# Kernel tuning notes

Hardware: AMD Instinct MI355X
Metric: run time of the kernel (lower is better)

## Reference

```python
import jax, jax.numpy as jnp
import numpy as np

PATCH_SIZE = 16
HOP_DISTANCE = 7.0


def setup_inputs() -> dict:
    key = jax.random.key(0)
    x = jax.random.normal(key, (1, 1024, 1024), dtype=jnp.float32)
    return {"x": x}


def _patchify(x, p):
    # Faithful replication of F.unfold(kernel=p, stride=p) followed by .view(-1, p, p)
    # on the contiguous [1, C*p*p, L] unfold output (row-major reshape).
    C, H, W = x.shape
    nH, nW = H // p, W // p
    # unfold layout: [C*p*p, L] with element (c*p*p + ki*p + kj, bi*nW + bj)
    cols = x.reshape(C, nH, p, nW, p).transpose(0, 2, 4, 1, 3).reshape(C * p * p, nH * nW)
    # torch .view(-1, p, p) on contiguous [C*p*p, L] == row-major reshape
    return cols.reshape(-1, p, p)  # [N, p, p], N = C * nH * nW


def reference(x):
    p = PATCH_SIZE
    patches = _patchify(x, p)  # [N, p, p]
    # distance(patch_i, patch_j) = norm over dim=1 (rows) -> per-column vector of length p.
    # d2[i, j, k] = sum_r (patches[i, r, k] - patches[j, r, k])**2, via Gram trick.
    sq = jnp.sum(patches * patches, axis=1)                      # [N, p]
    G = jnp.einsum('irk,jrk->ijk', patches, patches)             # [N, N, p]
    d2 = jnp.maximum(sq[:, None, :] + sq[None, :, :] - 2.0 * G, 0.0)
    # A[i, j] = 1 iff all per-column norms <= hop_distance
    A = jnp.all(jnp.sqrt(d2) <= HOP_DISTANCE, axis=-1).astype(jnp.float32)  # [N, N]
    return A
```

## Files before the change

kernel.cpp:

```cpp
#include <hip/hip_runtime.h>


#define NPATCH 4096
#define BT 64
#define KC 2
#define NPH 8

__global__ __launch_bounds__(128, 2) void adj_kernel(const float* __restrict__ x,
                                                     float* __restrict__ A) {
#pragma clang fp contract(off)
    __shared__ float4 Si[BT][8];
    __shared__ float4 Sj[BT][8];
    __shared__ float sqs[2][KC][BT];

    int t = blockIdx.x;
    int bi = (int)((sqrtf(8.0f * (float)t + 1.0f) - 1.0f) * 0.5f);
    while ((bi + 1) * (bi + 2) / 2 <= t) ++bi;
    while (bi * (bi + 1) / 2 > t) --bi;
    int bj = t - bi * (bi + 1) / 2;

    const int i0 = bi * BT;
    const int j0 = bj * BT;
    const int tid = threadIdx.x;
    const int tx = tid & 15;
    const int ty = tid >> 4;

    unsigned int bad = 0u;

    for (int kp = 0; kp < NPH; ++kp) {
        __syncthreads();
#pragma unroll
        for (int l = 0; l < 8; ++l) {
            int gid = l * 128 + tid;
            int side = gid >> 9;
            int q = gid & 511;
            int kl = q & 1;
            int r = (q >> 1) & 15;
            int rl = q >> 5;
            int k = kp * KC + kl;
            int b = side ? bj : bi;
            int h = rl * 64 + (r >> 2) * 16 + (b >> 2);
            int w0 = (r & 3) * 256 + k * 16 + ((4 * b) & 15);
            float4 v = *(const float4*)&x[h * 1024 + w0];
            const float* vp = (const float*)&v;
            int c = (kl << 2) | (r >> 2);
            int e = r & 3;
            float4* Sb = side ? &Sj[0][0] : &Si[0][0];
#pragma unroll
            for (int dd = 0; dd < 4; ++dd) {
                int row = 16 * dd + rl;
                int ch = c ^ ((row >> 2) & 7);
                ((float*)&Sb[row * 8 + ch])[e] = vp[dd];
            }
        }
        __syncthreads();
#pragma unroll
        for (int p = 0; p < 2; ++p) {
            int s0 = p * 128 + tid;
            int side = s0 >> 7;
            int kl = (s0 >> 6) & 1;
            int row = s0 & 63;
            const float4* Sb = side ? &Sj[row][0] : &Si[row][0];
            int swz = (row >> 2) & 7;
            float acc;
            {
                float4 v = Sb[(kl * 4) ^ swz];
                acc = v.x * v.x;
                float t1 = v.y * v.y; acc = acc + t1;
                float t2 = v.z * v.z; acc = acc + t2;
                float t3 = v.w * v.w; acc = acc + t3;
            }
#pragma unroll
            for (int rc = 1; rc < 4; ++rc) {
                float4 v = Sb[(kl * 4 + rc) ^ swz];
                float t0 = v.x * v.x; acc = acc + t0;
                float t1 = v.y * v.y; acc = acc + t1;
                float t2 = v.z * v.z; acc = acc + t2;
                float t3 = v.w * v.w; acc = acc + t3;
            }
            sqs[side][kl][row] = acc;
        }
        __syncthreads();
#pragma unroll
        for (int kl = 0; kl < KC; ++kl) {
            float d[8][4];
#pragma unroll
            for (int u = 0; u < 8; ++u)
#pragma unroll
                for (int v = 0; v < 4; ++v) d[u][v] = 0.0f;
#pragma unroll
            for (int rc = 0; rc < 4; ++rc) {
                int c = kl * 4 + rc;
                float4 a[8], b[4];
#pragma unroll
                for (int u = 0; u < 8; ++u)
                    a[u] = Si[ty * 8 + u][c ^ ((2 * ty + (u >> 2)) & 7)];
#pragma unroll
                for (int v = 0; v < 4; ++v)
                    b[v] = Sj[tx * 4 + v][c ^ (tx & 7)];
#pragma unroll
                for (int u = 0; u < 8; ++u)
#pragma unroll
                    for (int v = 0; v < 4; ++v) {
                        d[u][v] = fmaf(a[u].x, b[v].x, d[u][v]);
                        d[u][v] = fmaf(a[u].y, b[v].y, d[u][v]);
                        d[u][v] = fmaf(a[u].z, b[v].z, d[u][v]);
                        d[u][v] = fmaf(a[u].w, b[v].w, d[u][v]);
                    }
            }
#pragma unroll
            for (int u = 0; u < 8; ++u) {
                float si = sqs[0][kl][ty * 8 + u];
#pragma unroll
                for (int v = 0; v < 4; ++v) {
                    float sj = sqs[1][kl][tx * 4 + v];
                    float s = si + sj;
                    float d2 = fmaf(-2.0f, d[u][v], s);
                    bad |= (d2 > 49.0f) ? (1u << (u * 4 + v)) : 0u;
                }
            }
        }
    }

#pragma unroll
    for (int u = 0; u < 8; ++u) {
        float4 o;
        o.x = (bad >> (u * 4 + 0)) & 1u ? 0.0f : 1.0f;
        o.y = (bad >> (u * 4 + 1)) & 1u ? 0.0f : 1.0f;
        o.z = (bad >> (u * 4 + 2)) & 1u ? 0.0f : 1.0f;
        o.w = (bad >> (u * 4 + 3)) & 1u ? 0.0f : 1.0f;
        *(float4*)&A[(size_t)(i0 + ty * 8 + u) * NPATCH + j0 + tx * 4] = o;
    }
    if (bi != bj) {
#pragma unroll
        for (int v = 0; v < 4; ++v) {
#pragma unroll
            for (int g = 0; g < 2; ++g) {
                float4 o;
                o.x = (bad >> ((g * 4 + 0) * 4 + v)) & 1u ? 0.0f : 1.0f;
                o.y = (bad >> ((g * 4 + 1) * 4 + v)) & 1u ? 0.0f : 1.0f;
                o.z = (bad >> ((g * 4 + 2) * 4 + v)) & 1u ? 0.0f : 1.0f;
                o.w = (bad >> ((g * 4 + 3) * 4 + v)) & 1u ? 0.0f : 1.0f;
                *(float4*)&A[(size_t)(j0 + tx * 4 + v) * NPATCH + i0 + ty * 8 + g * 4] = o;
            }
        }
    }
}

extern "C" void kernel_launch(void* const* d_in, const int* in_sizes, int n_in,
                              void* d_out, int out_size, void* d_ws, size_t ws_size,
                              hipStream_t stream) {
    const float* x = (const float*)d_in[0];
    float* A = (float*)d_out;
    (void)d_ws; (void)ws_size;

    const int nblk = (NPATCH / BT) * (NPATCH / BT + 1) / 2;
    adj_kernel<<<nblk, 128, 0, stream>>>(x, A);
}
```

Before: 185.2 us.

## Use 128x64 rectangular tiles over the triangular block grid with 256 threads

Enlarges each block's tile to 128 i-rows by 64 j-columns, with 256 threads. Blocks are mapped onto a triangular grid of 64-row strip pairs against 64-column strips, with adjusted index math and shared arrays. Each block loads three patch strips and reuses the j strip across two i strips, which cuts per-output shared loads and the block count. The mirrored store now always runs, so diagonal blocks write some elements twice, once directly and once transposed. Bigger tiles mean fewer blocks, which can affect tail balance.

```diff
diff --git a/kernel.cpp b/kernel.cpp
--- a/kernel.cpp
+++ b/kernel.cpp
@@ -2,25 +2,25 @@
 
 
 #define NPATCH 4096
-#define BT 64
 #define KC 2
 #define NPH 8
 
-__global__ __launch_bounds__(128, 2) void adj_kernel(const float* __restrict__ x,
+__global__ __launch_bounds__(256, 2) void adj_kernel(const float* __restrict__ x,
                                                      float* __restrict__ A) {
 #pragma clang fp contract(off)
-    __shared__ float4 Si[BT][8];
-    __shared__ float4 Sj[BT][8];
-    __shared__ float sqs[2][KC][BT];
+    __shared__ float4 Si[128][8];
+    __shared__ float4 Sj[64][8];
+    __shared__ float sqi[KC][128];
+    __shared__ float sqj[KC][64];
 
     int t = blockIdx.x;
-    int bi = (int)((sqrtf(8.0f * (float)t + 1.0f) - 1.0f) * 0.5f);
-    while ((bi + 1) * (bi + 2) / 2 <= t) ++bi;
-    while (bi * (bi + 1) / 2 > t) --bi;
-    int bj = t - bi * (bi + 1) / 2;
+    int bi = (int)((sqrtf(4.0f * (float)t + 1.0f) - 1.0f) * 0.5f);
+    while ((bi + 1) * (bi + 2) > t) --bi;
+    while ((bi + 1) * (bi + 2) <= t) ++bi;
+    int bj = t - bi * (bi + 1);
 
-    const int i0 = bi * BT;
-    const int j0 = bj * BT;
+    const int i0 = bi * 128;
+    const int j0 = bj * 64;
     const int tid = threadIdx.x;
     const int tx = tid & 15;
     const int ty = tid >> 4;
@@ -30,22 +30,22 @@
     for (int kp = 0; kp < NPH; ++kp) {
         __syncthreads();
 #pragma unroll
-        for (int l = 0; l < 8; ++l) {
-            int gid = l * 128 + tid;
-            int side = gid >> 9;
+        for (int l = 0; l < 6; ++l) {
+            int gid = l * 256 + tid;
+            int strip = gid >> 9;
             int q = gid & 511;
             int kl = q & 1;
             int r = (q >> 1) & 15;
             int rl = q >> 5;
             int k = kp * KC + kl;
-            int b = side ? bj : bi;
+            int b = (strip == 2) ? bj : (2 * bi + strip);
             int h = rl * 64 + (r >> 2) * 16 + (b >> 2);
             int w0 = (r & 3) * 256 + k * 16 + ((4 * b) & 15);
             float4 v = *(const float4*)&x[h * 1024 + w0];
             const float* vp = (const float*)&v;
             int c = (kl << 2) | (r >> 2);
             int e = r & 3;
-            float4* Sb = side ? &Sj[0][0] : &Si[0][0];
+            float4* Sb = (strip == 2) ? &Sj[0][0] : &Si[(strip == 1) ? 64 : 0][0];
 #pragma unroll
             for (int dd = 0; dd < 4; ++dd) {
                 int row = 16 * dd + rl;
@@ -54,13 +54,13 @@
             }
         }
         __syncthreads();
-#pragma unroll
-        for (int p = 0; p < 2; ++p) {
-            int s0 = p * 128 + tid;
-            int side = s0 >> 7;
-            int kl = (s0 >> 6) & 1;
-            int row = s0 & 63;
-            const float4* Sb = side ? &Sj[row][0] : &Si[row][0];
+        for (int s0 = tid; s0 < 384; s0 += 256) {
+            int sideJ = (s0 >= 256);
+            int row, kl;
+            const float4* Sb;
+            float* dst;
+            if (!sideJ) { row = s0 & 127; kl = s0 >> 7; Sb = &Si[row][0]; dst = &sqi[kl][row]; }
+            else { int q = s0 - 256; row = q & 63; kl = q >> 6; Sb = &Sj[row][0]; dst = &sqj[kl][row]; }
             int swz = (row >> 2) & 7;
             float acc;
             {
@@ -78,7 +78,7 @@
                 float t2 = v.z * v.z; acc = acc + t2;
                 float t3 = v.w * v.w; acc = acc + t3;
             }
-            sqs[side][kl][row] = acc;
+            *dst = acc;
         }
         __syncthreads();
 #pragma unroll
@@ -110,10 +110,10 @@
             }
 #pragma unroll
             for (int u = 0; u < 8; ++u) {
-                float si = sqs[0][kl][ty * 8 + u];
+                float si = sqi[kl][ty * 8 + u];
 #pragma unroll
                 for (int v = 0; v < 4; ++v) {
-                    float sj = sqs[1][kl][tx * 4 + v];
+                    float sj = sqj[kl][tx * 4 + v];
                     float s = si + sj;
                     float d2 = fmaf(-2.0f, d[u][v], s);
                     bad |= (d2 > 49.0f) ? (1u << (u * 4 + v)) : 0u;
@@ -131,18 +131,16 @@
         o.w = (bad >> (u * 4 + 3)) & 1u ? 0.0f : 1.0f;
         *(float4*)&A[(size_t)(i0 + ty * 8 + u) * NPATCH + j0 + tx * 4] = o;
     }
-    if (bi != bj) {
 #pragma unroll
-        for (int v = 0; v < 4; ++v) {
+    for (int v = 0; v < 4; ++v) {
 #pragma unroll
-            for (int g = 0; g < 2; ++g) {
-                float4 o;
-                o.x = (bad >> ((g * 4 + 0) * 4 + v)) & 1u ? 0.0f : 1.0f;
-                o.y = (bad >> ((g * 4 + 1) * 4 + v)) & 1u ? 0.0f : 1.0f;
-                o.z = (bad >> ((g * 4 + 2) * 4 + v)) & 1u ? 0.0f : 1.0f;
-                o.w = (bad >> ((g * 4 + 3) * 4 + v)) & 1u ? 0.0f : 1.0f;
-                *(float4*)&A[(size_t)(j0 + tx * 4 + v) * NPATCH + i0 + ty * 8 + g * 4] = o;
-            }
+        for (int g = 0; g < 2; ++g) {
+            float4 o;
+            o.x = (bad >> ((g * 4 + 0) * 4 + v)) & 1u ? 0.0f : 1.0f;
+            o.y = (bad >> ((g * 4 + 1) * 4 + v)) & 1u ? 0.0f : 1.0f;
+            o.z = (bad >> ((g * 4 + 2) * 4 + v)) & 1u ? 0.0f : 1.0f;
+            o.w = (bad >> ((g * 4 + 3) * 4 + v)) & 1u ? 0.0f : 1.0f;
+            *(float4*)&A[(size_t)(j0 + tx * 4 + v) * NPATCH + i0 + ty * 8 + g * 4] = o;
         }
     }
 }
@@ -154,6 +152,6 @@
     float* A = (float*)d_out;
     (void)d_ws; (void)ws_size;
 
-    const int nblk = (NPATCH / BT) * (NPATCH / BT + 1) / 2;
-    adj_kernel<<<nblk, 128, 0, stream>>>(x, A);
+    const int nblk = 32 * 33;
+    adj_kernel<<<nblk, 256, 0, stream>>>(x, A);
 }
```

Result: no change. 182.0 us (-1.7%).
